# Kernel tuning notes

Measured on AMD Instinct MI355X. Metric: run time of the kernel, lower is better.

The kernel has to match this reference:

```python
import jax, jax.numpy as jnp
import numpy as np

N, E, P = 50000, 800000, 100000
IN, HID, H, L = 128, 128, 8, 3
D = HID // H


def setup_inputs() -> dict:
    key = jax.random.key(0)
    ks = jax.random.split(key, 24)
    rn = lambda k, shape, s: (jax.random.normal(k, shape, jnp.float32) * s)
    inp = {
        'x': jax.random.normal(ks[0], (N, IN), jnp.float32),
        'edge_src': jax.random.randint(ks[1], (E,), 0, N, jnp.int32),
        'edge_dst': jax.random.randint(ks[2], (E,), 0, N, jnp.int32),
        'edge_w': jax.random.uniform(ks[3], (E,), jnp.float32),
        'pos_src': jax.random.randint(ks[4], (P,), 0, N, jnp.int32),
        'pos_dst': jax.random.randint(ks[5], (P,), 0, N, jnp.int32),
        'neg_src': jax.random.randint(ks[6], (P,), 0, N, jnp.int32),
        'neg_dst': jax.random.randint(ks[7], (P,), 0, N, jnp.int32),
        # input projection
        'W_in': rn(ks[8], (IN, HID), IN ** -0.5),
        'b_in': jnp.zeros((HID,), jnp.float32),
        # per-layer HGT params (single ntype/etype -> plain matrices)
        'Wk': rn(ks[9], (L, HID, HID), HID ** -0.5),
        'Wq': rn(ks[10], (L, HID, HID), HID ** -0.5),
        'Wv': rn(ks[11], (L, HID, HID), HID ** -0.5),
        'att_w': rn(ks[12], (L, H, D, D), D ** -0.5),
        'msg_w': rn(ks[13], (L, H, D, D), D ** -0.5),
        'pri': jnp.ones((L, H), jnp.float32),
        'Wa': rn(ks[14], (L, HID, HID), HID ** -0.5),
        'skip': jnp.ones((L,), jnp.float32),
        # predictor MLP
        'W1': rn(ks[15], (HID, HID // 2), HID ** -0.5),
        'b1': jnp.zeros((HID // 2,), jnp.float32),
        'W2': rn(ks[16], (HID // 2, HID // 4), (HID // 2) ** -0.5),
        'b2': jnp.zeros((HID // 4,), jnp.float32),
        'W3': rn(ks[17], (HID // 4, 1), (HID // 4) ** -0.5),
        'b3': jnp.zeros((1,), jnp.float32),
    }
    return inp


def _hgt_forward(x, edge_src, edge_dst, edge_w, pos_src, pos_dst, neg_src, neg_dst,
                 W_in, b_in, Wk, Wq, Wv, att_w, msg_w, pri, Wa, skip,
                 W1, b1, W2, b2, W3, b3):
    n = x.shape[0]
    nheads = att_w.shape[1]
    d = att_w.shape[2]
    sqrt_d = jnp.asarray(d ** 0.5, x.dtype)
    h = jax.nn.relu(x @ W_in + b_in)
    nlayers = Wk.shape[0]
    for l in range(nlayers):
        k = (h @ Wk[l]).reshape(n, nheads, d)
        q = (h @ Wq[l]).reshape(n, nheads, d)
        v = (h @ Wv[l]).reshape(n, nheads, d)
        # relation-specific per-head transforms (etype constant -> node-level)
        kw = jnp.einsum('nhd,hde->nhe', k, att_w[l])
        mv = jnp.einsum('nhd,hde->nhe', v, msg_w[l])
        # per-edge attention logits [E, H]
        a = (kw[edge_src] * q[edge_dst]).sum(-1) * pri[l] / sqrt_d
        # edge softmax grouped by destination node
        amax = jax.ops.segment_max(a, edge_dst, num_segments=n)[edge_dst]
        ex = jnp.exp(a - amax)
        denom = jax.ops.segment_sum(ex, edge_dst, num_segments=n)[edge_dst]
        attn = ex / denom
        # weighted messages + scatter-sum  [E,H,D] -> [N,H,D]
        m = mv[edge_src] * edge_w[:, None, None] * attn[:, :, None]
        agg = jax.ops.segment_sum(m, edge_dst, num_segments=n).reshape(n, nheads * d)
        hn = agg @ Wa[l]  # linear_a (dropout is identity in eval)
        alpha = jax.nn.sigmoid(skip[l])
        h = hn * alpha + h * (1.0 - alpha)
        if l != nlayers - 1:
            h = jax.nn.relu(h)  # inter-layer relu (dropout identity)
    def predictor(z):
        z = jax.nn.leaky_relu(z @ W1 + b1, 0.2)
        z = jax.nn.leaky_relu(z @ W2 + b2, 0.2)
        return z @ W3 + b3
    h_pos = predictor(h[pos_src] * h[pos_dst])
    h_neg = predictor(h[neg_src] * h[neg_dst])
    return h_pos, h_neg, h


def reference(x, edge_src, edge_dst, edge_w, pos_src, pos_dst, neg_src, neg_dst,
              W_in, b_in, Wk, Wq, Wv, att_w, msg_w, pri, Wa, skip,
              W1, b1, W2, b2, W3, b3):
    return _hgt_forward(x, edge_src, edge_dst, edge_w, pos_src, pos_dst,
                        neg_src, neg_dst, W_in, b_in, Wk, Wq, Wv, att_w,
                        msg_w, pri, Wa, skip, W1, b1, W2, b2, W3, b3)
```

## Files before the change

### kernel.cpp

```cpp
#include <hip/hip_runtime.h>
#include <cstddef>

#define N_NODES 50000
#define N_EDGES 800000
#define N_PAIRS 100000

typedef float floatx4 __attribute__((ext_vector_type(4)));
typedef _Float16 half2v __attribute__((ext_vector_type(2)));
typedef _Float16 half4v __attribute__((ext_vector_type(4)));
typedef _Float16 half8v __attribute__((ext_vector_type(8)));

__device__ inline size_t packA(int m, int k, int K) {
  return ((size_t)((m >> 4) * (K >> 5) + (k >> 5)) << 9) +
         ((((unsigned)k >> 3) & 3) << 7) + ((m & 15) << 3) + (k & 7);
}
__device__ inline void store_h8(_Float16* __restrict__ dst, size_t base, const float* vals) {
  half8v hv;
#pragma unroll
  for (int i = 0; i < 8; i++) hv[i] = (_Float16)vals[i];
  *(half8v*)(dst + base) = hv;
}

__device__ inline float fold_val(int l, int r, int j, const float* Wk, const float* Wq,
                                 const float* Wv, const float* att, const float* msg,
                                 const float* pri) {
  if (j >= 128 && j < 256) return Wq[(l * 128 + r) * 128 + (j - 128)];
  int jj = j & 127, hh = jj >> 4, e = jj & 15;
  const float* W = (j < 128) ? Wk : Wv;
  const float* T = (j < 128) ? att : msg;
  float s = 0.f;
#pragma unroll
  for (int d = 0; d < 16; d++)
    s += W[(l * 128 + r) * 128 + hh * 16 + d] * T[((l * 8 + hh) * 16 + d) * 16 + e];
  if (j < 128) s *= pri[l * 8 + hh] * 0.25f;
  return s;
}

__global__ void wprep_kernel(const float* __restrict__ W_in, const float* __restrict__ Wk,
                             const float* __restrict__ Wq, const float* __restrict__ Wv,
                             const float* __restrict__ att, const float* __restrict__ msg,
                             const float* __restrict__ pri, const float* __restrict__ Wa,
                             const float* __restrict__ W1, const float* __restrict__ W2,
                             _Float16* Wint, _Float16* Wcat, _Float16* Waf,
                             _Float16* W1f, _Float16* W2f) {
  int gid = blockIdx.x * 256 + threadIdx.x;
  float v;
  _Float16* dt;
  size_t o;
  if (gid < 16384) {
    int n = gid >> 7, k = gid & 127;
    v = W_in[k * 128 + n];
    dt = Wint; o = packA(n, k, 128);
  } else if (gid < 163840) {
    int t = gid - 16384;
    int l = t / 49152, u = t - l * 49152;
    int n = u >> 7, k = u & 127;
    v = fold_val(l, k, n, Wk, Wq, Wv, att, msg, pri);
    dt = Wcat + (size_t)l * 49152;
    o = packA(n, k, 128);
  } else if (gid < 212992) {
    int t = gid - 163840;
    int l = t / 16384, u = t & 16383;
    int n = u >> 7, k = u & 127;
    v = Wa[(size_t)l * 16384 + k * 128 + n];
    dt = Waf + (size_t)l * 16384;
    o = packA(n, k, 128);
  } else if (gid < 221184) {
    int u = gid - 212992;
    int n = u >> 7, k = u & 127;
    v = W1[k * 64 + n];
    dt = W1f; o = packA(n, k, 128);
  } else if (gid < 225280) {
    int u = gid - 221184;
    int n = u >> 6, k = u & 63;
    v = (n < 32) ? W2[k * 32 + n] : 0.f;
    dt = W2f; o = packA(n, k, 64);
  } else {
    return;
  }
  dt[o] = (_Float16)v;
}

__global__ void hist_kernel(const int* __restrict__ dst, int* __restrict__ deg, int E) {
  int g = blockIdx.x * blockDim.x + threadIdx.x;
  if (g < E) atomicAdd(&deg[dst[g]], 1);
}

__global__ void scanA_kernel(const int* __restrict__ deg, int* __restrict__ offs,
                             int* __restrict__ bsum, int n) {
  __shared__ int sm[256];
  int t = threadIdx.x;
  int i = blockIdx.x * 256 + t;
  int v = (i < n) ? ((deg[i] + 15) & ~15) : 0;
  sm[t] = v;
  __syncthreads();
  for (int off = 1; off < 256; off <<= 1) {
    int u = (t >= off) ? sm[t - off] : 0;
    __syncthreads();
    sm[t] += u;
    __syncthreads();
  }
  if (i < n) offs[i] = sm[t] - v;
  if (t == 255) bsum[blockIdx.x] = sm[255];
}

__global__ void scanB_kernel(const int* __restrict__ bsum, int* __restrict__ boff,
                             int* __restrict__ offs, int nb, int n) {
  __shared__ int sm[256];
  int t = threadIdx.x;
  int v = (t < nb) ? bsum[t] : 0;
  sm[t] = v;
  __syncthreads();
  for (int off = 1; off < 256; off <<= 1) {
    int u = (t >= off) ? sm[t - off] : 0;
    __syncthreads();
    sm[t] += u;
    __syncthreads();
  }
  boff[t] = sm[t] - v;
  if (t == nb - 1) offs[n] = sm[t];
}

__global__ void scanC_kernel(int* __restrict__ offs, const int* __restrict__ boff,
                             int* __restrict__ cursor, int n) {
  int i = blockIdx.x * 256 + threadIdx.x;
  if (i < n) {
    int o = offs[i] + boff[blockIdx.x];
    offs[i] = o;
    cursor[i] = o;
  }
}

__global__ void scatter_kernel(const int* __restrict__ src, const int* __restrict__ dst,
                               const float* __restrict__ w, int* __restrict__ cursor,
                               int2* __restrict__ eld, int E) {
  int g = blockIdx.x * blockDim.x + threadIdx.x;
  if (g < E) {
    int d = dst[g];
    int p = atomicAdd(&cursor[d], 1);
    eld[p] = make_int2(src[g], __float_as_int(w[g]));
  }
}

__global__ void bhist_kernel(const int* __restrict__ deg, int* __restrict__ bh, int n) {
  __shared__ int lh[256];
  int t = threadIdx.x;
  lh[t] = 0;
  __syncthreads();
  int i = blockIdx.x * 256 + t;
  if (i < n) atomicAdd(&lh[min(deg[i], 255)], 1);
  __syncthreads();
  if (lh[t]) atomicAdd(&bh[t], lh[t]);
}
__global__ void bscan_kernel(const int* __restrict__ bh, int* __restrict__ bcur) {
  __shared__ int sm[256];
  int t = threadIdx.x;
  int v = bh[255 - t];
  sm[t] = v;
  __syncthreads();
  for (int off = 1; off < 256; off <<= 1) {
    int u = (t >= off) ? sm[t - off] : 0;
    __syncthreads();
    sm[t] += u;
    __syncthreads();
  }
  bcur[255 - t] = sm[t] - v;
}
__global__ void bscatter_kernel(const int* __restrict__ deg, int* __restrict__ bcur,
                                int* __restrict__ perm, int n) {
  __shared__ int lh[256], lbase[256];
  int t = threadIdx.x;
  lh[t] = 0;
  __syncthreads();
  int i = blockIdx.x * 256 + t;
  int b = 0, local = 0;
  if (i < n) {
    b = min(deg[i], 255);
    local = atomicAdd(&lh[b], 1);
  }
  __syncthreads();
  int cnt = lh[t];
  lbase[t] = cnt ? atomicAdd(&bcur[t], cnt) : 0;
  __syncthreads();
  if (i < n) perm[lbase[b] + local] = i;
}

template <int AMODE>
__global__ __launch_bounds__(256) void gemm_mfma(
    const _Float16* __restrict__ Ah, const float* __restrict__ Af,
    const _Float16* __restrict__ hrow_src,
    const int* __restrict__ psrc, const int* __restrict__ pdst,
    const int* __restrict__ nsrc, const int* __restrict__ ndst,
    const _Float16* __restrict__ Bt,
    int M, int N, int K, int epi,
    const float* __restrict__ bias, const _Float16* __restrict__ hold,
    const float* __restrict__ skipv, int relu,
    float* __restrict__ Cf, _Float16* __restrict__ Ch, int Kout,
    const float* __restrict__ W3, const float* __restrict__ b3,
    float* __restrict__ outd, _Float16* __restrict__ kwmv, _Float16* __restrict__ qbuf,
    _Float16* __restrict__ hrow_out) {
  int tid = threadIdx.x;
  int wave = tid >> 6, lane = tid & 63;
  int l16 = lane & 15, q = lane >> 4;
  int m_base = blockIdx.x * 128 + wave * 32;
  int n_base = blockIdx.y * 64;
  int kc_count = K >> 5;

  bool tv[2];
  int pa[2], pb[2], rowA[2];
  size_t a_base[2];
#pragma unroll
  for (int mt = 0; mt < 2; mt++) {
    int tile = (m_base >> 4) + mt;
    tv[mt] = (tile * 16) < M;
    if (AMODE == 0) {
      a_base[mt] = (size_t)(tv[mt] ? tile : 0) * ((size_t)kc_count << 9) + lane * 8;
    } else if (AMODE == 1) {
      rowA[mt] = min(m_base + mt * 16 + l16, M - 1);
    } else {
      int gr = min(m_base + mt * 16 + l16, M - 1);
      bool pos = gr < N_PAIRS;
      int idx = pos ? gr : gr - N_PAIRS;
      pa[mt] = pos ? psrc[idx] : nsrc[idx];
      pb[mt] = pos ? pdst[idx] : ndst[idx];
    }
  }

  half8v a[2][4];
#pragma unroll
  for (int kc = 0; kc < 4; kc++) {
    if (kc >= kc_count) break;
    int kbase = kc * 32 + q * 8;
#pragma unroll
    for (int mt = 0; mt < 2; mt++) {
      if (AMODE == 0) {
        a[mt][kc] = tv[mt] ? *(const half8v*)(Ah + a_base[mt] + (kc << 9))
                           : (half8v)(_Float16)0.f;
      } else if (AMODE == 1) {
        const float* p = Af + (size_t)rowA[mt] * K + kbase;
        float4 u0 = *(const float4*)p, u1 = *(const float4*)(p + 4);
        float f[8] = {u0.x, u0.y, u0.z, u0.w, u1.x, u1.y, u1.z, u1.w};
        half8v hv;
#pragma unroll
        for (int i = 0; i < 8; i++) hv[i] = (_Float16)f[i];
        a[mt][kc] = hv;
      } else {
        half8v ha = *(const half8v*)(hrow_src + (size_t)pa[mt] * 128 + kbase);
        half8v hb = *(const half8v*)(hrow_src + (size_t)pb[mt] * 128 + kbase);
        a[mt][kc] = ha * hb;
      }
    }
  }

  floatx4 acc[2][4];
#pragma unroll
  for (int i = 0; i < 2; i++)
#pragma unroll
    for (int j = 0; j < 4; j++) acc[i][j] = (floatx4){0.f, 0.f, 0.f, 0.f};
  size_t bb[4];
#pragma unroll
  for (int nt = 0; nt < 4; nt++)
    bb[nt] = (size_t)((n_base >> 4) + nt) * ((size_t)kc_count << 9) + lane * 8;
#pragma unroll
  for (int kc = 0; kc < 4; kc++) {
    if (kc >= kc_count) break;
    half8v b[4];
#pragma unroll
    for (int nt = 0; nt < 4; nt++) b[nt] = *(const half8v*)(Bt + bb[nt] + (kc << 9));
#pragma unroll
    for (int mt = 0; mt < 2; mt++)
#pragma unroll
      for (int nt = 0; nt < 4; nt++)
        acc[mt][nt] = __builtin_amdgcn_mfma_f32_16x16x32_f16(a[mt][kc], b[nt],
                                                             acc[mt][nt], 0, 0, 0);
  }

  if (epi == 4) {
    float b3v = b3[0];
    float bw[4], wv[4];
#pragma unroll
    for (int nt = 0; nt < 4; nt++) {
      int col = n_base + nt * 16 + l16;
      bool inb = col < N;
      bw[nt] = inb ? bias[col] : 0.f;
      wv[nt] = inb ? W3[col] : 0.f;
    }
#pragma unroll
    for (int mt = 0; mt < 2; mt++) {
      if (!tv[mt]) continue;
#pragma unroll
      for (int r = 0; r < 4; r++) {
        float partial = 0.f;
#pragma unroll
        for (int nt = 0; nt < 4; nt++) {
          float v = acc[mt][nt][r] + bw[nt];
          v = v > 0.f ? v : 0.2f * v;
          partial += v * wv[nt];
        }
        partial += __shfl_xor(partial, 1);
        partial += __shfl_xor(partial, 2);
        partial += __shfl_xor(partial, 4);
        partial += __shfl_xor(partial, 8);
        int row = m_base + mt * 16 + q * 4 + r;
        if (l16 == 0 && row < M) outd[row] = partial + b3v;
      }
    }
    return;
  }

  __shared__ float ldsT[4][16 * 68];
  float* myT = &ldsT[wave][0];
  float alpha = 1.f, beta = 0.f;
  if (epi == 2) {
    float sv = *skipv;
    alpha = 1.f / (1.f + __expf(-sv));
    beta = 1.f - alpha;
  }
  int g = lane >> 4, mloc = lane & 15;
#pragma unroll
  for (int mt = 0; mt < 2; mt++) {
    int row0 = m_base + mt * 16;
#pragma unroll
    for (int nt = 0; nt < 4; nt++)
#pragma unroll
      for (int r = 0; r < 4; r++)
        myT[(q * 4 + r) * 68 + nt * 16 + l16] = acc[mt][nt][r];
    __syncthreads();
    if (tv[mt]) {
      int row = row0 + mloc;
#pragma unroll
      for (int kc2 = 0; kc2 < 2; kc2++) {
        const float* rp = myT + mloc * 68 + kc2 * 32 + g * 8;
        floatx4 v0 = *(const floatx4*)rp;
        floatx4 v1 = *(const floatx4*)(rp + 4);
        float vals[8] = {v0[0], v0[1], v0[2], v0[3], v1[0], v1[1], v1[2], v1[3]};
        int col0 = n_base + kc2 * 32 + g * 8;
        size_t pbase = ((size_t)((row0 >> 4) * (Kout >> 5) + (col0 >> 5)) << 9) +
                       (size_t)lane * 8;
        if (epi == 0) {
          float4 bb0 = *(const float4*)&bias[col0];
          float4 bb1 = *(const float4*)&bias[col0 + 4];
          float bbv[8] = {bb0.x, bb0.y, bb0.z, bb0.w, bb1.x, bb1.y, bb1.z, bb1.w};
#pragma unroll
          for (int j = 0; j < 8; j++) vals[j] = fmaxf(vals[j] + bbv[j], 0.f);
          store_h8(Ch, pbase, vals);
        } else if (epi == 1) {
          int region = col0 >> 7;
          if (region == 1) {
            half8v hv;
#pragma unroll
            for (int j = 0; j < 8; j++) hv[j] = (_Float16)vals[j];
            *(half8v*)&qbuf[(size_t)row * 128 + (col0 - 128)] = hv;
          } else {
            int cc = col0 & 127;
            size_t base = (size_t)row * 256 + (size_t)(cc >> 2) * 8 +
                          (region == 2 ? 4 : 0);
            half4v h0, h1;
#pragma unroll
            for (int j = 0; j < 4; j++) {
              h0[j] = (_Float16)vals[j];
              h1[j] = (_Float16)vals[j + 4];
            }
            *(half4v*)&kwmv[base] = h0;
            *(half4v*)&kwmv[base + 8] = h1;
          }
        } else if (epi == 2) {
          half8v hv = *(const half8v*)(hold + pbase);
#pragma unroll
          for (int j = 0; j < 8; j++) {
            vals[j] = alpha * vals[j] + beta * (float)hv[j];
            if (relu) vals[j] = fmaxf(vals[j], 0.f);
          }
          if (Cf) {
            *(float4*)&Cf[(size_t)row * N + col0] =
                make_float4(vals[0], vals[1], vals[2], vals[3]);
            *(float4*)&Cf[(size_t)row * N + col0 + 4] =
                make_float4(vals[4], vals[5], vals[6], vals[7]);
          }
          if (Ch) store_h8(Ch, pbase, vals);
          if (hrow_out) store_h8(hrow_out, (size_t)row * 128 + col0, vals);
        } else {
          float4 bb0 = *(const float4*)&bias[col0];
          float4 bb1 = *(const float4*)&bias[col0 + 4];
          float bbv[8] = {bb0.x, bb0.y, bb0.z, bb0.w, bb1.x, bb1.y, bb1.z, bb1.w};
#pragma unroll
          for (int j = 0; j < 8; j++) {
            float v = vals[j] + bbv[j];
            vals[j] = v > 0.f ? v : 0.2f * v;
          }
          store_h8(Ch, pbase, vals);
        }
      }
    }
    __syncthreads();
  }
}

__global__ __launch_bounds__(256) void edge_agg_kernel(
    const _Float16* __restrict__ kwmv, const _Float16* __restrict__ qbuf,
    const int* __restrict__ poffs, const int2* __restrict__ eld,
    const int* __restrict__ perm,
    _Float16* __restrict__ agg, int n) {
  int wslot = blockIdx.x * 4 + (threadIdx.x >> 6);
  int lane = threadIdx.x & 63;
  int hh = lane >> 5;
  int c4 = lane & 31;
  int ch = c4 << 2;
  for (int gw = wslot; gw < n; gw += 8192) {
    int node = perm[gw];
    half4v qv = *(const half4v*)&qbuf[(size_t)node * 128 + ch];
    half2v q01 = {qv[0], qv[1]}, q23 = {qv[2], qv[3]};
    float m = -1e30f, s = 0.f;
    float a0 = 0.f, a1 = 0.f, a2 = 0.f, a3 = 0.f;
    int beg = poffs[node], end = poffs[node + 1];
    for (int j = beg; j < end; j += 16) {
      int2 e[8];
      half8v kvmv[8];
#pragma unroll
      for (int i = 0; i < 8; i++) {
        e[i] = eld[j + 2 * i + hh];
        kvmv[i] = *(const half8v*)&kwmv[(size_t)max(e[i].x, 0) * 256 + (size_t)c4 * 8];
      }
      float p[8];
#pragma unroll
      for (int i = 0; i < 8; i++) {
        half2v k01 = {kvmv[i][0], kvmv[i][1]}, k23 = {kvmv[i][2], kvmv[i][3]};
        float d = __builtin_amdgcn_fdot2(
            k01, q01, __builtin_amdgcn_fdot2(k23, q23, 0.f, false), false);
        d += __shfl_xor(d, 1);
        d += __shfl_xor(d, 2);
        p[i] = (e[i].x >= 0) ? d : -1e30f;
      }
      float nm = m;
#pragma unroll
      for (int i = 0; i < 8; i++) nm = fmaxf(nm, p[i]);
      float sc = __expf(m - nm);
      float t[8];
      float ssum = 0.f;
#pragma unroll
      for (int i = 0; i < 8; i++) {
        t[i] = __expf(p[i] - nm);
        ssum += t[i];
      }
      s = s * sc + ssum;
      a0 *= sc; a1 *= sc; a2 *= sc; a3 *= sc;
#pragma unroll
      for (int i = 0; i < 8; i++) {
        float w = (e[i].x >= 0) ? __int_as_float(e[i].y) : 0.f;
        float f = t[i] * w;
        a0 += f * (float)kvmv[i][4];
        a1 += f * (float)kvmv[i][5];
        a2 += f * (float)kvmv[i][6];
        a3 += f * (float)kvmv[i][7];
      }
      m = nm;
    }
    float mo = __shfl_xor(m, 32);
    float so = __shfl_xor(s, 32);
    float c0 = __shfl_xor(a0, 32), c1 = __shfl_xor(a1, 32);
    float c2 = __shfl_xor(a2, 32), c3 = __shfl_xor(a3, 32);
    float M = fmaxf(m, mo);
    float e1 = __expf(m - M), e2 = __expf(mo - M);
    float st = s * e1 + so * e2;
    float v0 = a0 * e1 + c0 * e2, v1 = a1 * e1 + c1 * e2;
    float v2 = a2 * e1 + c2 * e2, v3 = a3 * e1 + c3 * e2;
    float inv = (st > 0.f) ? 1.f / st : 0.f;
    if (hh == 0) {
      half4v out4;
      out4[0] = (_Float16)(v0 * inv);
      out4[1] = (_Float16)(v1 * inv);
      out4[2] = (_Float16)(v2 * inv);
      out4[3] = (_Float16)(v3 * inv);
      *(half4v*)&agg[packA(node, ch, 128)] = out4;
    }
  }
}

extern "C" void kernel_launch(void* const* d_in, const int* in_sizes, int n_in,
                              void* d_out, int out_size, void* d_ws, size_t ws_size,
                              hipStream_t stream) {
  const float* x        = (const float*)d_in[0];
  const int*   edge_src = (const int*)d_in[1];
  const int*   edge_dst = (const int*)d_in[2];
  const float* edge_w   = (const float*)d_in[3];
  const int*   pos_src  = (const int*)d_in[4];
  const int*   pos_dst  = (const int*)d_in[5];
  const int*   neg_src  = (const int*)d_in[6];
  const int*   neg_dst  = (const int*)d_in[7];
  const float* W_in     = (const float*)d_in[8];
  const float* b_in     = (const float*)d_in[9];
  const float* Wk       = (const float*)d_in[10];
  const float* Wq       = (const float*)d_in[11];
  const float* Wv       = (const float*)d_in[12];
  const float* att_w    = (const float*)d_in[13];
  const float* msg_w    = (const float*)d_in[14];
  const float* pri      = (const float*)d_in[15];
  const float* Wa       = (const float*)d_in[16];
  const float* skip     = (const float*)d_in[17];
  const float* W1       = (const float*)d_in[18];
  const float* b1       = (const float*)d_in[19];
  const float* W2       = (const float*)d_in[20];
  const float* b2       = (const float*)d_in[21];
  const float* W3       = (const float*)d_in[22];
  const float* b3       = (const float*)d_in[23];
  float* out = (float*)d_out;

  char* W = (char*)d_ws;
  _Float16*  qbuf   = (_Float16*)(W + 0);
  _Float16*  kwmv   = (_Float16*)(W + 12800000);
  _Float16*  hbuf   = (_Float16*)(W + 38400000);
  _Float16*  agg    = (_Float16*)(W + 51200000);
  _Float16*  Wint   = (_Float16*)(W + 64000000);
  _Float16*  Wcat   = (_Float16*)(W + 64032768);
  _Float16*  Waf    = (_Float16*)(W + 64327680);
  _Float16*  W1f    = (_Float16*)(W + 64425984);
  _Float16*  W2f    = (_Float16*)(W + 64442368);
  int2*      eld    = (int2*)(W + 64450560);
  int*       deg    = (int*)(W + 77250560);
  int*       poffs  = (int*)(W + 77450560);
  int*       cursor = (int*)(W + 77650576);
  int*       perm   = (int*)(W + 77850576);
  int*       bsum   = (int*)(W + 78050576);
  int*       boff   = (int*)(W + 78051600);
  int*       bh     = (int*)(W + 78052624);
  int*       bcur   = (int*)(W + 78053648);
  _Float16*  hrow   = (_Float16*)(W + 78054912);
  _Float16* T1 = (_Float16*)(W + 0);
  float* hfinal = out + 2 * N_PAIRS;

  hipMemsetAsync(deg, 0, N_NODES * sizeof(int), stream);
  hipMemsetAsync(bh, 0, 1024, stream);
  hipMemsetAsync(eld, 0xFF, 12800000, stream);

  wprep_kernel<<<880, 256, 0, stream>>>(W_in, Wk, Wq, Wv, att_w, msg_w, pri, Wa, W1, W2,
                                        Wint, Wcat, Waf, W1f, W2f);
  hist_kernel<<<(N_EDGES + 255) / 256, 256, 0, stream>>>(edge_dst, deg, N_EDGES);
  scanA_kernel<<<196, 256, 0, stream>>>(deg, poffs, bsum, N_NODES);
  scanB_kernel<<<1, 256, 0, stream>>>(bsum, boff, poffs, 196, N_NODES);
  scanC_kernel<<<196, 256, 0, stream>>>(poffs, boff, cursor, N_NODES);
  scatter_kernel<<<(N_EDGES + 255) / 256, 256, 0, stream>>>(
      edge_src, edge_dst, edge_w, cursor, eld, N_EDGES);
  bhist_kernel<<<196, 256, 0, stream>>>(deg, bh, N_NODES);
  bscan_kernel<<<1, 256, 0, stream>>>(bh, bcur);
  bscatter_kernel<<<196, 256, 0, stream>>>(deg, bcur, perm, N_NODES);

  gemm_mfma<1><<<dim3(391, 2), 256, 0, stream>>>(
      nullptr, x, nullptr, nullptr, nullptr, nullptr, nullptr,
      Wint, N_NODES, 128, 128, 0, b_in, nullptr, nullptr, 0,
      nullptr, hbuf, 128, nullptr, nullptr, nullptr, nullptr, nullptr, nullptr);

  for (int l = 0; l < 3; l++) {
    gemm_mfma<0><<<dim3(391, 6), 256, 0, stream>>>(
        hbuf, nullptr, nullptr, nullptr, nullptr, nullptr, nullptr,
        Wcat + l * 49152, N_NODES, 384, 128, 1, nullptr, nullptr, nullptr, 0,
        nullptr, nullptr, 128, nullptr, nullptr, nullptr, kwmv, qbuf, nullptr);
    edge_agg_kernel<<<2048, 256, 0, stream>>>(
        kwmv, qbuf, poffs, eld, perm, agg, N_NODES);
    int last = (l == 2);
    gemm_mfma<0><<<dim3(391, 2), 256, 0, stream>>>(
        agg, nullptr, nullptr, nullptr, nullptr, nullptr, nullptr,
        Waf + l * 16384, N_NODES, 128, 128, 2, nullptr, hbuf, skip + l,
        last ? 0 : 1, last ? hfinal : nullptr, last ? nullptr : hbuf, 128,
        nullptr, nullptr, nullptr, nullptr, nullptr, last ? hrow : nullptr);
  }

  gemm_mfma<2><<<dim3(1563, 1), 256, 0, stream>>>(
      nullptr, nullptr, hrow, pos_src, pos_dst, neg_src, neg_dst,
      W1f, 2 * N_PAIRS, 64, 128, 3, b1, nullptr, nullptr, 0,
      nullptr, T1, 64, nullptr, nullptr, nullptr, nullptr, nullptr, nullptr);
  gemm_mfma<0><<<dim3(1563, 1), 256, 0, stream>>>(
      T1, nullptr, nullptr, nullptr, nullptr, nullptr, nullptr,
      W2f, 2 * N_PAIRS, 32, 64, 4, b2, nullptr, nullptr, 0,
      nullptr, nullptr, 64, W3, b3, out, nullptr, nullptr, nullptr);
}
```

Baseline: 602.4 us.

## Fuse per-layer GEMM chains and predictor MLP into single kernels

Replaces the generic templated GEMM with specialized kernels. Each kernel fuses the output projection and skip mix of one layer with the next layer's K/Q/V projection, keeping the 16-row h tile in LDS. The two predictor GEMMs plus the final dot product now run in one kernel, so the T1 intermediate never goes to global memory. This cuts kernel launches and global round trips of the intermediates, at the cost of more LDS and registers per block and each wave handling a full 16x384 output strip.

Result: faster. 561.5 us (-6.8%).

```diff
diff --git a/kernel.cpp b/kernel.cpp
--- a/kernel.cpp
+++ b/kernel.cpp
@@ -13,12 +13,6 @@
 __device__ inline size_t packA(int m, int k, int K) {
   return ((size_t)((m >> 4) * (K >> 5) + (k >> 5)) << 9) +
          ((((unsigned)k >> 3) & 3) << 7) + ((m & 15) << 3) + (k & 7);
-}
-__device__ inline void store_h8(_Float16* __restrict__ dst, size_t base, const float* vals) {
-  half8v hv;
-#pragma unroll
-  for (int i = 0; i < 8; i++) hv[i] = (_Float16)vals[i];
-  *(half8v*)(dst + base) = hv;
 }
 
 __device__ inline float fold_val(int l, int r, int j, const float* Wk, const float* Wq,
@@ -185,214 +179,347 @@
   if (i < n) perm[lbase[b] + local] = i;
 }
 
-template <int AMODE>
-__global__ __launch_bounds__(256) void gemm_mfma(
-    const _Float16* __restrict__ Ah, const float* __restrict__ Af,
-    const _Float16* __restrict__ hrow_src,
-    const int* __restrict__ psrc, const int* __restrict__ pdst,
-    const int* __restrict__ nsrc, const int* __restrict__ ndst,
-    const _Float16* __restrict__ Bt,
-    int M, int N, int K, int epi,
-    const float* __restrict__ bias, const _Float16* __restrict__ hold,
-    const float* __restrict__ skipv, int relu,
-    float* __restrict__ Cf, _Float16* __restrict__ Ch, int Kout,
-    const float* __restrict__ W3, const float* __restrict__ b3,
-    float* __restrict__ outd, _Float16* __restrict__ kwmv, _Float16* __restrict__ qbuf,
-    _Float16* __restrict__ hrow_out) {
+template <int FIRST>
+__global__ __launch_bounds__(256) void fused_layer(
+    const float* __restrict__ x, const _Float16* __restrict__ aggp,
+    const _Float16* __restrict__ Wg1, const float* __restrict__ bias,
+    const float* __restrict__ skipv, _Float16* __restrict__ hbuf,
+    const _Float16* __restrict__ Wcat_l,
+    _Float16* __restrict__ kwmv, _Float16* __restrict__ qbuf, int M) {
   int tid = threadIdx.x;
   int wave = tid >> 6, lane = tid & 63;
   int l16 = lane & 15, q = lane >> 4;
-  int m_base = blockIdx.x * 128 + wave * 32;
-  int n_base = blockIdx.y * 64;
-  int kc_count = K >> 5;
-
-  bool tv[2];
-  int pa[2], pb[2], rowA[2];
-  size_t a_base[2];
-#pragma unroll
-  for (int mt = 0; mt < 2; mt++) {
-    int tile = (m_base >> 4) + mt;
-    tv[mt] = (tile * 16) < M;
-    if (AMODE == 0) {
-      a_base[mt] = (size_t)(tv[mt] ? tile : 0) * ((size_t)kc_count << 9) + lane * 8;
-    } else if (AMODE == 1) {
-      rowA[mt] = min(m_base + mt * 16 + l16, M - 1);
+  int g = q, mloc = l16;
+  int tile = blockIdx.x * 4 + wave;
+  int m0 = tile * 16;
+  bool alive = m0 < M;
+  int tileC = alive ? tile : 0;
+
+  __shared__ _Float16 htile_s[4][2048];
+  __shared__ float ldsT_s[4][16 * 68];
+  _Float16* htile = htile_s[wave];
+  float* myT = ldsT_s[wave];
+
+  half8v a[4];
+#pragma unroll
+  for (int kc = 0; kc < 4; kc++) {
+    if (FIRST) {
+      int row = min(m0 + l16, M - 1);
+      const float* p = x + (size_t)row * 128 + kc * 32 + q * 8;
+      float4 u0 = *(const float4*)p, u1 = *(const float4*)(p + 4);
+      float f[8] = {u0.x, u0.y, u0.z, u0.w, u1.x, u1.y, u1.z, u1.w};
+      half8v hv;
+#pragma unroll
+      for (int i = 0; i < 8; i++) hv[i] = (_Float16)f[i];
+      a[kc] = hv;
     } else {
-      int gr = min(m_base + mt * 16 + l16, M - 1);
-      bool pos = gr < N_PAIRS;
-      int idx = pos ? gr : gr - N_PAIRS;
-      pa[mt] = pos ? psrc[idx] : nsrc[idx];
-      pb[mt] = pos ? pdst[idx] : ndst[idx];
-    }
-  }
-
-  half8v a[2][4];
-#pragma unroll
-  for (int kc = 0; kc < 4; kc++) {
-    if (kc >= kc_count) break;
-    int kbase = kc * 32 + q * 8;
-#pragma unroll
-    for (int mt = 0; mt < 2; mt++) {
-      if (AMODE == 0) {
-        a[mt][kc] = tv[mt] ? *(const half8v*)(Ah + a_base[mt] + (kc << 9))
-                           : (half8v)(_Float16)0.f;
-      } else if (AMODE == 1) {
-        const float* p = Af + (size_t)rowA[mt] * K + kbase;
-        float4 u0 = *(const float4*)p, u1 = *(const float4*)(p + 4);
-        float f[8] = {u0.x, u0.y, u0.z, u0.w, u1.x, u1.y, u1.z, u1.w};
-        half8v hv;
-#pragma unroll
-        for (int i = 0; i < 8; i++) hv[i] = (_Float16)f[i];
-        a[mt][kc] = hv;
-      } else {
-        half8v ha = *(const half8v*)(hrow_src + (size_t)pa[mt] * 128 + kbase);
-        half8v hb = *(const half8v*)(hrow_src + (size_t)pb[mt] * 128 + kbase);
-        a[mt][kc] = ha * hb;
-      }
-    }
-  }
-
-  floatx4 acc[2][4];
-#pragma unroll
-  for (int i = 0; i < 2; i++)
-#pragma unroll
-    for (int j = 0; j < 4; j++) acc[i][j] = (floatx4){0.f, 0.f, 0.f, 0.f};
-  size_t bb[4];
-#pragma unroll
-  for (int nt = 0; nt < 4; nt++)
-    bb[nt] = (size_t)((n_base >> 4) + nt) * ((size_t)kc_count << 9) + lane * 8;
-#pragma unroll
-  for (int kc = 0; kc < 4; kc++) {
-    if (kc >= kc_count) break;
-    half8v b[4];
-#pragma unroll
-    for (int nt = 0; nt < 4; nt++) b[nt] = *(const half8v*)(Bt + bb[nt] + (kc << 9));
-#pragma unroll
-    for (int mt = 0; mt < 2; mt++)
-#pragma unroll
-      for (int nt = 0; nt < 4; nt++)
-        acc[mt][nt] = __builtin_amdgcn_mfma_f32_16x16x32_f16(a[mt][kc], b[nt],
-                                                             acc[mt][nt], 0, 0, 0);
-  }
-
-  if (epi == 4) {
-    float b3v = b3[0];
-    float bw[4], wv[4];
-#pragma unroll
-    for (int nt = 0; nt < 4; nt++) {
-      int col = n_base + nt * 16 + l16;
-      bool inb = col < N;
-      bw[nt] = inb ? bias[col] : 0.f;
-      wv[nt] = inb ? W3[col] : 0.f;
-    }
-#pragma unroll
-    for (int mt = 0; mt < 2; mt++) {
-      if (!tv[mt]) continue;
-#pragma unroll
-      for (int r = 0; r < 4; r++) {
-        float partial = 0.f;
-#pragma unroll
-        for (int nt = 0; nt < 4; nt++) {
-          float v = acc[mt][nt][r] + bw[nt];
-          v = v > 0.f ? v : 0.2f * v;
-          partial += v * wv[nt];
-        }
-        partial += __shfl_xor(partial, 1);
-        partial += __shfl_xor(partial, 2);
-        partial += __shfl_xor(partial, 4);
-        partial += __shfl_xor(partial, 8);
-        int row = m_base + mt * 16 + q * 4 + r;
-        if (l16 == 0 && row < M) outd[row] = partial + b3v;
-      }
-    }
-    return;
-  }
-
-  __shared__ float ldsT[4][16 * 68];
-  float* myT = &ldsT[wave][0];
+      a[kc] = *(const half8v*)(aggp + (size_t)tileC * 2048 + (kc << 9) + lane * 8);
+    }
+  }
+
   float alpha = 1.f, beta = 0.f;
-  if (epi == 2) {
+  if (!FIRST) {
     float sv = *skipv;
     alpha = 1.f / (1.f + __expf(-sv));
     beta = 1.f - alpha;
   }
-  int g = lane >> 4, mloc = lane & 15;
-#pragma unroll
-  for (int mt = 0; mt < 2; mt++) {
-    int row0 = m_base + mt * 16;
-#pragma unroll
-    for (int nt = 0; nt < 4; nt++)
+
+  floatx4 acc1[8];
+#pragma unroll
+  for (int nt = 0; nt < 8; nt++) acc1[nt] = (floatx4){0.f, 0.f, 0.f, 0.f};
+#pragma unroll
+  for (int kc = 0; kc < 4; kc++) {
+    half8v b[8];
+#pragma unroll
+    for (int nt = 0; nt < 8; nt++)
+      b[nt] = *(const half8v*)(Wg1 + (size_t)nt * 2048 + (kc << 9) + lane * 8);
+#pragma unroll
+    for (int nt = 0; nt < 8; nt++)
+      acc1[nt] = __builtin_amdgcn_mfma_f32_16x16x32_f16(a[kc], b[nt], acc1[nt], 0, 0, 0);
+  }
+
+#pragma unroll
+  for (int p = 0; p < 2; p++) {
+    __syncthreads();
+#pragma unroll
+    for (int ntl = 0; ntl < 4; ntl++)
 #pragma unroll
       for (int r = 0; r < 4; r++)
-        myT[(q * 4 + r) * 68 + nt * 16 + l16] = acc[mt][nt][r];
-    __syncthreads();
-    if (tv[mt]) {
-      int row = row0 + mloc;
+        myT[(q * 4 + r) * 68 + ntl * 16 + l16] = acc1[p * 4 + ntl][r];
+    __syncthreads();
+#pragma unroll
+    for (int kc2 = 0; kc2 < 2; kc2++) {
+      const float* rp = myT + mloc * 68 + kc2 * 32 + g * 8;
+      floatx4 v0 = *(const floatx4*)rp;
+      floatx4 v1 = *(const floatx4*)(rp + 4);
+      float vals[8] = {v0[0], v0[1], v0[2], v0[3], v1[0], v1[1], v1[2], v1[3]};
+      int col0 = p * 64 + kc2 * 32 + g * 8;
+      size_t pbaseL = ((size_t)(tileC * 4 + (col0 >> 5)) << 9) + (size_t)lane * 8;
+      if (FIRST) {
+        float4 bb0 = *(const float4*)&bias[col0];
+        float4 bb1 = *(const float4*)&bias[col0 + 4];
+        float bbv[8] = {bb0.x, bb0.y, bb0.z, bb0.w, bb1.x, bb1.y, bb1.z, bb1.w};
+#pragma unroll
+        for (int j = 0; j < 8; j++) vals[j] = fmaxf(vals[j] + bbv[j], 0.f);
+      } else {
+        half8v hv = *(const half8v*)(hbuf + pbaseL);
+#pragma unroll
+        for (int j = 0; j < 8; j++)
+          vals[j] = fmaxf(alpha * vals[j] + beta * (float)hv[j], 0.f);
+      }
+      half8v h8;
+#pragma unroll
+      for (int j = 0; j < 8; j++) h8[j] = (_Float16)vals[j];
+      *(half8v*)(htile + (((p * 2 + kc2) << 9) + (g << 7) + (mloc << 3))) = h8;
+      if (alive) *(half8v*)(hbuf + pbaseL) = h8;
+    }
+  }
+
+  for (int c = 0; c < 6; c++) {
+    floatx4 acc2[4];
+#pragma unroll
+    for (int nt = 0; nt < 4; nt++) acc2[nt] = (floatx4){0.f, 0.f, 0.f, 0.f};
+#pragma unroll
+    for (int kc = 0; kc < 4; kc++) {
+      half8v af = *(const half8v*)(htile + ((kc << 9) + lane * 8));
+      half8v b[4];
+#pragma unroll
+      for (int nt = 0; nt < 4; nt++)
+        b[nt] = *(const half8v*)(Wcat_l + (size_t)(c * 4 + nt) * 2048 + (kc << 9) + lane * 8);
+#pragma unroll
+      for (int nt = 0; nt < 4; nt++)
+        acc2[nt] = __builtin_amdgcn_mfma_f32_16x16x32_f16(af, b[nt], acc2[nt], 0, 0, 0);
+    }
+    __syncthreads();
+#pragma unroll
+    for (int ntl = 0; ntl < 4; ntl++)
+#pragma unroll
+      for (int r = 0; r < 4; r++)
+        myT[(q * 4 + r) * 68 + ntl * 16 + l16] = acc2[ntl][r];
+    __syncthreads();
+    if (alive) {
+      int row = m0 + mloc;
+#pragma unroll
+      for (int kc2 = 0; kc2 < 2; kc2++) {
+        const float* rp = myT + mloc * 68 + kc2 * 32 + g * 8;
+        floatx4 v0 = *(const floatx4*)rp;
+        floatx4 v1 = *(const floatx4*)(rp + 4);
+        int col0 = c * 64 + kc2 * 32 + g * 8;
+        int region = col0 >> 7;
+        if (region == 1) {
+          half8v h8;
+#pragma unroll
+          for (int j = 0; j < 4; j++) {
+            h8[j] = (_Float16)v0[j];
+            h8[j + 4] = (_Float16)v1[j];
+          }
+          *(half8v*)&qbuf[(size_t)row * 128 + (col0 - 128)] = h8;
+        } else {
+          int cc = col0 & 127;
+          size_t base = (size_t)row * 256 + (size_t)(cc >> 2) * 8 + (region == 2 ? 4 : 0);
+          half4v h0, h1;
+#pragma unroll
+          for (int j = 0; j < 4; j++) {
+            h0[j] = (_Float16)v0[j];
+            h1[j] = (_Float16)v1[j];
+          }
+          *(half4v*)&kwmv[base] = h0;
+          *(half4v*)&kwmv[base + 8] = h1;
+        }
+      }
+    }
+  }
+}
+
+__global__ __launch_bounds__(256) void gemm_last(
+    const _Float16* __restrict__ aggp, const _Float16* __restrict__ Wg1,
+    const float* __restrict__ skipv, const _Float16* __restrict__ hbuf,
+    float* __restrict__ hfinal, _Float16* __restrict__ hrow, int M) {
+  int tid = threadIdx.x;
+  int wave = tid >> 6, lane = tid & 63;
+  int l16 = lane & 15, q = lane >> 4;
+  int g = q, mloc = l16;
+  int tile = blockIdx.x * 4 + wave;
+  int m0 = tile * 16;
+  bool alive = m0 < M;
+  int tileC = alive ? tile : 0;
+
+  __shared__ float ldsT_s[4][16 * 68];
+  float* myT = ldsT_s[wave];
+
+  half8v a[4];
+#pragma unroll
+  for (int kc = 0; kc < 4; kc++)
+    a[kc] = *(const half8v*)(aggp + (size_t)tileC * 2048 + (kc << 9) + lane * 8);
+
+  float sv = *skipv;
+  float alpha = 1.f / (1.f + __expf(-sv));
+  float beta = 1.f - alpha;
+
+  floatx4 acc1[8];
+#pragma unroll
+  for (int nt = 0; nt < 8; nt++) acc1[nt] = (floatx4){0.f, 0.f, 0.f, 0.f};
+#pragma unroll
+  for (int kc = 0; kc < 4; kc++) {
+    half8v b[8];
+#pragma unroll
+    for (int nt = 0; nt < 8; nt++)
+      b[nt] = *(const half8v*)(Wg1 + (size_t)nt * 2048 + (kc << 9) + lane * 8);
+#pragma unroll
+    for (int nt = 0; nt < 8; nt++)
+      acc1[nt] = __builtin_amdgcn_mfma_f32_16x16x32_f16(a[kc], b[nt], acc1[nt], 0, 0, 0);
+  }
+
+#pragma unroll
+  for (int p = 0; p < 2; p++) {
+    __syncthreads();
+#pragma unroll
+    for (int ntl = 0; ntl < 4; ntl++)
+#pragma unroll
+      for (int r = 0; r < 4; r++)
+        myT[(q * 4 + r) * 68 + ntl * 16 + l16] = acc1[p * 4 + ntl][r];
+    __syncthreads();
+    if (alive) {
+      int row = m0 + mloc;
 #pragma unroll
       for (int kc2 = 0; kc2 < 2; kc2++) {
         const float* rp = myT + mloc * 68 + kc2 * 32 + g * 8;
         floatx4 v0 = *(const floatx4*)rp;
         floatx4 v1 = *(const floatx4*)(rp + 4);
         float vals[8] = {v0[0], v0[1], v0[2], v0[3], v1[0], v1[1], v1[2], v1[3]};
-        int col0 = n_base + kc2 * 32 + g * 8;
-        size_t pbase = ((size_t)((row0 >> 4) * (Kout >> 5) + (col0 >> 5)) << 9) +
-                       (size_t)lane * 8;
-        if (epi == 0) {
-          float4 bb0 = *(const float4*)&bias[col0];
-          float4 bb1 = *(const float4*)&bias[col0 + 4];
-          float bbv[8] = {bb0.x, bb0.y, bb0.z, bb0.w, bb1.x, bb1.y, bb1.z, bb1.w};
-#pragma unroll
-          for (int j = 0; j < 8; j++) vals[j] = fmaxf(vals[j] + bbv[j], 0.f);
-          store_h8(Ch, pbase, vals);
-        } else if (epi == 1) {
-          int region = col0 >> 7;
-          if (region == 1) {
-            half8v hv;
-#pragma unroll
-            for (int j = 0; j < 8; j++) hv[j] = (_Float16)vals[j];
-            *(half8v*)&qbuf[(size_t)row * 128 + (col0 - 128)] = hv;
-          } else {
-            int cc = col0 & 127;
-            size_t base = (size_t)row * 256 + (size_t)(cc >> 2) * 8 +
-                          (region == 2 ? 4 : 0);
-            half4v h0, h1;
-#pragma unroll
-            for (int j = 0; j < 4; j++) {
-              h0[j] = (_Float16)vals[j];
-              h1[j] = (_Float16)vals[j + 4];
-            }
-            *(half4v*)&kwmv[base] = h0;
-            *(half4v*)&kwmv[base + 8] = h1;
-          }
-        } else if (epi == 2) {
-          half8v hv = *(const half8v*)(hold + pbase);
-#pragma unroll
-          for (int j = 0; j < 8; j++) {
-            vals[j] = alpha * vals[j] + beta * (float)hv[j];
-            if (relu) vals[j] = fmaxf(vals[j], 0.f);
-          }
-          if (Cf) {
-            *(float4*)&Cf[(size_t)row * N + col0] =
-                make_float4(vals[0], vals[1], vals[2], vals[3]);
-            *(float4*)&Cf[(size_t)row * N + col0 + 4] =
-                make_float4(vals[4], vals[5], vals[6], vals[7]);
-          }
-          if (Ch) store_h8(Ch, pbase, vals);
-          if (hrow_out) store_h8(hrow_out, (size_t)row * 128 + col0, vals);
-        } else {
-          float4 bb0 = *(const float4*)&bias[col0];
-          float4 bb1 = *(const float4*)&bias[col0 + 4];
-          float bbv[8] = {bb0.x, bb0.y, bb0.z, bb0.w, bb1.x, bb1.y, bb1.z, bb1.w};
-#pragma unroll
-          for (int j = 0; j < 8; j++) {
-            float v = vals[j] + bbv[j];
-            vals[j] = v > 0.f ? v : 0.2f * v;
-          }
-          store_h8(Ch, pbase, vals);
-        }
+        int col0 = p * 64 + kc2 * 32 + g * 8;
+        size_t pbase = ((size_t)(tile * 4 + (col0 >> 5)) << 9) + (size_t)lane * 8;
+        half8v hv = *(const half8v*)(hbuf + pbase);
+#pragma unroll
+        for (int j = 0; j < 8; j++) vals[j] = alpha * vals[j] + beta * (float)hv[j];
+        *(float4*)&hfinal[(size_t)row * 128 + col0] =
+            make_float4(vals[0], vals[1], vals[2], vals[3]);
+        *(float4*)&hfinal[(size_t)row * 128 + col0 + 4] =
+            make_float4(vals[4], vals[5], vals[6], vals[7]);
+        half8v h8;
+#pragma unroll
+        for (int j = 0; j < 8; j++) h8[j] = (_Float16)vals[j];
+        *(half8v*)&hrow[(size_t)row * 128 + col0] = h8;
       }
     }
-    __syncthreads();
+  }
+}
+
+__global__ __launch_bounds__(256) void pred_fused(
+    const _Float16* __restrict__ hrow,
+    const int* __restrict__ ps, const int* __restrict__ pd,
+    const int* __restrict__ ns, const int* __restrict__ nd,
+    const _Float16* __restrict__ W1f, const float* __restrict__ b1,
+    const _Float16* __restrict__ W2f, const float* __restrict__ b2,
+    const float* __restrict__ W3, const float* __restrict__ b3,
+    float* __restrict__ outd, int M) {
+  int tid = threadIdx.x;
+  int wave = tid >> 6, lane = tid & 63;
+  int l16 = lane & 15, q = lane >> 4;
+  int g = q, mloc = l16;
+  int tile = blockIdx.x * 4 + wave;
+  int m0 = tile * 16;
+  bool alive = m0 < M;
+
+  __shared__ _Float16 t1_s[4][1024];
+  __shared__ float ldsT_s[4][16 * 68];
+  _Float16* t1tile = t1_s[wave];
+  float* myT = ldsT_s[wave];
+
+  int gr = min(m0 + l16, M - 1);
+  bool pos = gr < N_PAIRS;
+  int idx = pos ? gr : gr - N_PAIRS;
+  int pa = pos ? ps[idx] : ns[idx];
+  int pb = pos ? pd[idx] : nd[idx];
+
+  half8v a[4];
+#pragma unroll
+  for (int kc = 0; kc < 4; kc++) {
+    int kbase = kc * 32 + q * 8;
+    half8v ha = *(const half8v*)(hrow + (size_t)pa * 128 + kbase);
+    half8v hb = *(const half8v*)(hrow + (size_t)pb * 128 + kbase);
+    a[kc] = ha * hb;
+  }
+
+  floatx4 acc1[4];
+#pragma unroll
+  for (int nt = 0; nt < 4; nt++) acc1[nt] = (floatx4){0.f, 0.f, 0.f, 0.f};
+#pragma unroll
+  for (int kc = 0; kc < 4; kc++) {
+    half8v b[4];
+#pragma unroll
+    for (int nt = 0; nt < 4; nt++)
+      b[nt] = *(const half8v*)(W1f + (size_t)nt * 2048 + (kc << 9) + lane * 8);
+#pragma unroll
+    for (int nt = 0; nt < 4; nt++)
+      acc1[nt] = __builtin_amdgcn_mfma_f32_16x16x32_f16(a[kc], b[nt], acc1[nt], 0, 0, 0);
+  }
+
+  __syncthreads();
+#pragma unroll
+  for (int ntl = 0; ntl < 4; ntl++)
+#pragma unroll
+    for (int r = 0; r < 4; r++)
+      myT[(q * 4 + r) * 68 + ntl * 16 + l16] = acc1[ntl][r];
+  __syncthreads();
+#pragma unroll
+  for (int kc2 = 0; kc2 < 2; kc2++) {
+    const float* rp = myT + mloc * 68 + kc2 * 32 + g * 8;
+    floatx4 v0 = *(const floatx4*)rp;
+    floatx4 v1 = *(const floatx4*)(rp + 4);
+    float vals[8] = {v0[0], v0[1], v0[2], v0[3], v1[0], v1[1], v1[2], v1[3]};
+    int col0 = kc2 * 32 + g * 8;
+    float4 bb0 = *(const float4*)&b1[col0];
+    float4 bb1 = *(const float4*)&b1[col0 + 4];
+    float bbv[8] = {bb0.x, bb0.y, bb0.z, bb0.w, bb1.x, bb1.y, bb1.z, bb1.w};
+    half8v h8;
+#pragma unroll
+    for (int j = 0; j < 8; j++) {
+      float v = vals[j] + bbv[j];
+      v = v > 0.f ? v : 0.2f * v;
+      h8[j] = (_Float16)v;
+    }
+    *(half8v*)(t1tile + ((kc2 << 9) + (g << 7) + (mloc << 3))) = h8;
+  }
+
+  floatx4 acc2[2];
+#pragma unroll
+  for (int nt = 0; nt < 2; nt++) acc2[nt] = (floatx4){0.f, 0.f, 0.f, 0.f};
+#pragma unroll
+  for (int kc = 0; kc < 2; kc++) {
+    half8v af = *(const half8v*)(t1tile + ((kc << 9) + lane * 8));
+    half8v b[2];
+#pragma unroll
+    for (int nt = 0; nt < 2; nt++)
+      b[nt] = *(const half8v*)(W2f + (size_t)nt * 1024 + (kc << 9) + lane * 8);
+#pragma unroll
+    for (int nt = 0; nt < 2; nt++)
+      acc2[nt] = __builtin_amdgcn_mfma_f32_16x16x32_f16(af, b[nt], acc2[nt], 0, 0, 0);
+  }
+
+  float bw[2], wv[2];
+#pragma unroll
+  for (int nt = 0; nt < 2; nt++) {
+    int col = nt * 16 + l16;
+    bw[nt] = b2[col];
+    wv[nt] = W3[col];
+  }
+  float b3v = b3[0];
+#pragma unroll
+  for (int r = 0; r < 4; r++) {
+    float partial = 0.f;
+#pragma unroll
+    for (int nt = 0; nt < 2; nt++) {
+      float v = acc2[nt][r] + bw[nt];
+      v = v > 0.f ? v : 0.2f * v;
+      partial += v * wv[nt];
+    }
+    partial += __shfl_xor(partial, 1);
+    partial += __shfl_xor(partial, 2);
+    partial += __shfl_xor(partial, 4);
+    partial += __shfl_xor(partial, 8);
+    int row = m0 + q * 4 + r;
+    if (l16 == 0 && alive && row < M) outd[row] = partial + b3v;
   }
 }
 
@@ -525,7 +652,6 @@
   int*       bh     = (int*)(W + 78052624);
   int*       bcur   = (int*)(W + 78053648);
   _Float16*  hrow   = (_Float16*)(W + 78054912);
-  _Float16* T1 = (_Float16*)(W + 0);
   float* hfinal = out + 2 * N_PAIRS;
 
   hipMemsetAsync(deg, 0, N_NODES * sizeof(int), stream);
@@ -544,32 +670,17 @@
   bscan_kernel<<<1, 256, 0, stream>>>(bh, bcur);
   bscatter_kernel<<<196, 256, 0, stream>>>(deg, bcur, perm, N_NODES);
 
-  gemm_mfma<1><<<dim3(391, 2), 256, 0, stream>>>(
-      nullptr, x, nullptr, nullptr, nullptr, nullptr, nullptr,
-      Wint, N_NODES, 128, 128, 0, b_in, nullptr, nullptr, 0,
-      nullptr, hbuf, 128, nullptr, nullptr, nullptr, nullptr, nullptr, nullptr);
-
-  for (int l = 0; l < 3; l++) {
-    gemm_mfma<0><<<dim3(391, 6), 256, 0, stream>>>(
-        hbuf, nullptr, nullptr, nullptr, nullptr, nullptr, nullptr,
-        Wcat + l * 49152, N_NODES, 384, 128, 1, nullptr, nullptr, nullptr, 0,
-        nullptr, nullptr, 128, nullptr, nullptr, nullptr, kwmv, qbuf, nullptr);
-    edge_agg_kernel<<<2048, 256, 0, stream>>>(
-        kwmv, qbuf, poffs, eld, perm, agg, N_NODES);
-    int last = (l == 2);
-    gemm_mfma<0><<<dim3(391, 2), 256, 0, stream>>>(
-        agg, nullptr, nullptr, nullptr, nullptr, nullptr, nullptr,
-        Waf + l * 16384, N_NODES, 128, 128, 2, nullptr, hbuf, skip + l,
-        last ? 0 : 1, last ? hfinal : nullptr, last ? nullptr : hbuf, 128,
-        nullptr, nullptr, nullptr, nullptr, nullptr, last ? hrow : nullptr);
-  }
-
-  gemm_mfma<2><<<dim3(1563, 1), 256, 0, stream>>>(
-      nullptr, nullptr, hrow, pos_src, pos_dst, neg_src, neg_dst,
-      W1f, 2 * N_PAIRS, 64, 128, 3, b1, nullptr, nullptr, 0,
-      nullptr, T1, 64, nullptr, nullptr, nullptr, nullptr, nullptr, nullptr);
-  gemm_mfma<0><<<dim3(1563, 1), 256, 0, stream>>>(
-      T1, nullptr, nullptr, nullptr, nullptr, nullptr, nullptr,
-      W2f, 2 * N_PAIRS, 32, 64, 4, b2, nullptr, nullptr, 0,
-      nullptr, nullptr, 64, W3, b3, out, nullptr, nullptr, nullptr);
-}
+  fused_layer<1><<<782, 256, 0, stream>>>(x, nullptr, Wint, b_in, nullptr, hbuf,
+                                          Wcat, kwmv, qbuf, N_NODES);
+  edge_agg_kernel<<<2048, 256, 0, stream>>>(kwmv, qbuf, poffs, eld, perm, agg, N_NODES);
+  fused_layer<0><<<782, 256, 0, stream>>>(nullptr, agg, Waf, nullptr, skip + 0, hbuf,
+                                          Wcat + 49152, kwmv, qbuf, N_NODES);
+  edge_agg_kernel<<<2048, 256, 0, stream>>>(kwmv, qbuf, poffs, eld, perm, agg, N_NODES);
+  fused_layer<0><<<782, 256, 0, stream>>>(nullptr, agg, Waf + 16384, nullptr, skip + 1,
+                                          hbuf, Wcat + 98304, kwmv, qbuf, N_NODES);
+  edge_agg_kernel<<<2048, 256, 0, stream>>>(kwmv, qbuf, poffs, eld, perm, agg, N_NODES);
+  gemm_last<<<782, 256, 0, stream>>>(agg, Waf + 32768, skip + 2, hbuf,
+                                     hfinal, hrow, N_NODES);
+  pred_fused<<<3125, 256, 0, stream>>>(hrow, pos_src, pos_dst, neg_src, neg_dst,
+                                       W1f, b1, W2f, b2, W3, b3, out, 2 * N_PAIRS);
+}
```
